# Performance work log

Hardware: AMD Instinct MI355X
Metric: run time of the kernel (lower is better)

Reference implementation:

```python
import jax, jax.numpy as jnp
import numpy as np

N, IN_DIM, OUT_DIM = 8192, 128, 64
NEG_INF = -9e15

def setup_inputs() -> dict:
    key = jax.random.key(0)
    k1, k2, k3, k4 = jax.random.split(key, 4)
    h = jax.random.normal(k1, (N, IN_DIM), dtype=jnp.float32)
    adj = jax.random.randint(k2, (N, N), 0, 2, dtype=jnp.int32)
    W = jax.random.normal(k3, (IN_DIM, OUT_DIM), dtype=jnp.float32) * (1.0 / np.sqrt(IN_DIM))
    a = jax.random.normal(k4, (2 * OUT_DIM,), dtype=jnp.float32)
    return {"h": h, "adj": adj, "W": W, "a": a}

def reference(h, adj, W, a):
    Wh = h @ W  # [N, F]
    F_ = Wh.shape[1]
    # additive decomposition of cat([Wh_i, Wh_j]) @ a == Wh_i@a1 + Wh_j@a2
    e_src = Wh @ a[:F_]   # [N]
    e_dst = Wh @ a[F_:]   # [N]
    e = jax.nn.leaky_relu(e_src[:, None] + e_dst[None, :], negative_slope=0.01)  # [N, N]
    attention = jnp.where(adj > 0, e, jnp.float32(NEG_INF))
    attention = jax.nn.softmax(attention, axis=1)
    h_prime = attention @ Wh  # [N, F]
    return jax.nn.elu(h_prime)
```

## Files before the change

### kernel.cpp

```cpp
#include <hip/hip_runtime.h>
#include <hip/hip_bf16.h>

typedef __attribute__((ext_vector_type(8))) short short8;
typedef __attribute__((ext_vector_type(4))) float f32x4;

#define NROW 8192
#define FDIM 64
#define INDIM 128
#define BM 128
#define SPLITS 16
#define NPANEL (NROW / BM)
#define MBOUND 48.0f
#define L2E 1.44269504f

static __device__ __forceinline__ unsigned short bfb(float x) {
  __hip_bfloat16 b = __float2bfloat16(x);
  return *reinterpret_cast<unsigned short*>(&b);
}
static __device__ __forceinline__ float b2f(unsigned int u16) {
  unsigned int x = u16 << 16;
  float f;
  __builtin_memcpy(&f, &x, 4);
  return f;
}
static __device__ __forceinline__ float lrelu(float x) { return fmaxf(x, 0.01f * x); }

__global__ __launch_bounds__(256) void k_wh(const float* __restrict__ h,
                                            const float* __restrict__ W,
                                            const float* __restrict__ a,
                                            __hip_bfloat16* __restrict__ WhT,
                                            float* __restrict__ s,
                                            float* __restrict__ d) {
  const int i = blockIdx.x * 4 + (threadIdx.x >> 6);
  const int f = threadIdx.x & 63;
  const float* hrow = h + (size_t)i * INDIM;
  float acc = 0.f;
#pragma unroll 8
  for (int k = 0; k < INDIM; ++k) acc = fmaf(hrow[k], W[k * FDIM + f], acc);
  WhT[(size_t)f * NROW + i] = __float2bfloat16(acc);
  float p1 = acc * a[f];
  float p2 = acc * a[FDIM + f];
#pragma unroll
  for (int m = 32; m; m >>= 1) {
    p1 += __shfl_xor(p1, m, 64);
    p2 += __shfl_xor(p2, m, 64);
  }
  if (f == 0) { s[i] = p1; d[i] = p2; }
}

__global__ __launch_bounds__(256, 4) void k_main(const int* __restrict__ adj,
                                                 const __hip_bfloat16* __restrict__ WhT,
                                                 const float* __restrict__ sArr,
                                                 const float* __restrict__ dArr,
                                                 unsigned int* __restrict__ accp,
                                                 float* __restrict__ Zp) {
  const int t = threadIdx.x;
  const int w = t >> 6, l = t & 63;
  const int lr = l & 15;
  const int lk = l >> 4;
  const int panel = blockIdx.x / SPLITS;
  const int split = blockIdx.x - panel * SPLITS;
  const int row0 = panel * BM + w * 32;
  const int jspan = NROW / SPLITS;
  const int j0 = split * jspan;
  const int nchunk = jspan / 64;

  const float s0 = sArr[row0 + lr];
  const float s1 = sArr[row0 + 16 + lr];
  const float sm0 = -lrelu(s0 + MBOUND) * L2E;
  const float sm1 = -lrelu(s1 + MBOUND) * L2E;

  f32x4 acc[2][4];
#pragma unroll
  for (int ri = 0; ri < 2; ++ri)
#pragma unroll
    for (int nf = 0; nf < 4; ++nf) acc[ri][nf] = (f32x4){0.f, 0.f, 0.f, 0.f};
  float z0 = 0.f, z1 = 0.f;

  const int* adjp = adj + (size_t)row0 * NROW + j0 + l;
  const float* dp = dArr + j0 + lk * 8;
  const __hip_bfloat16* bbase = WhT + (size_t)lr * NROW + j0 + lk * 8;

  for (int c = 0; c < nchunk; ++c) {
    const int off = c * 64;

    unsigned long long M0 = 0ull, M1 = 0ull;
    {
      int av[16];
#pragma unroll
      for (int r = 0; r < 16; ++r) av[r] = adjp[(size_t)r * NROW + off];
#pragma unroll
      for (int r = 0; r < 16; ++r) {
        unsigned long long b = __ballot(av[r] > 0);
        M0 = (lr == r) ? b : M0;
      }
#pragma unroll
      for (int r = 0; r < 16; ++r) av[r] = adjp[(size_t)(16 + r) * NROW + off];
#pragma unroll
      for (int r = 0; r < 16; ++r) {
        unsigned long long b = __ballot(av[r] > 0);
        M1 = (lr == r) ? b : M1;
      }
    }

#pragma unroll
    for (int ks = 0; ks < 2; ++ks) {
      const int jo = off + ks * 32;
      const unsigned int y0 = (unsigned int)(M0 >> (ks * 32 + lk * 8)) & 0xffu;
      const unsigned int y1 = (unsigned int)(M1 >> (ks * 32 + lk * 8)) & 0xffu;

      short8 b0 = *(const short8*)(bbase + jo);
      short8 b1 = *(const short8*)(bbase + jo + 16 * NROW);
      short8 b2 = *(const short8*)(bbase + jo + 32 * NROW);
      short8 b3 = *(const short8*)(bbase + jo + 48 * NROW);

      float dj[8];
      *(float4*)&dj[0] = *(const float4*)(dp + jo);
      *(float4*)&dj[4] = *(const float4*)(dp + jo + 4);

      short8 pa0, pa1;
#pragma unroll
      for (int q = 0; q < 8; ++q) {
        const float dq = dj[q];
        float e0 = exp2f(fmaf(lrelu(s0 + dq), L2E, sm0));
        float e1 = exp2f(fmaf(lrelu(s1 + dq), L2E, sm1));
        float w0 = ((y0 >> q) & 1u) ? e0 : 0.f;
        float w1 = ((y1 >> q) & 1u) ? e1 : 0.f;
        z0 += w0;
        z1 += w1;
        pa0[q] = (short)bfb(w0);
        pa1[q] = (short)bfb(w1);
      }

      acc[0][0] = __builtin_amdgcn_mfma_f32_16x16x32_bf16(pa0, b0, acc[0][0], 0, 0, 0);
      acc[0][1] = __builtin_amdgcn_mfma_f32_16x16x32_bf16(pa0, b1, acc[0][1], 0, 0, 0);
      acc[0][2] = __builtin_amdgcn_mfma_f32_16x16x32_bf16(pa0, b2, acc[0][2], 0, 0, 0);
      acc[0][3] = __builtin_amdgcn_mfma_f32_16x16x32_bf16(pa0, b3, acc[0][3], 0, 0, 0);
      acc[1][0] = __builtin_amdgcn_mfma_f32_16x16x32_bf16(pa1, b0, acc[1][0], 0, 0, 0);
      acc[1][1] = __builtin_amdgcn_mfma_f32_16x16x32_bf16(pa1, b1, acc[1][1], 0, 0, 0);
      acc[1][2] = __builtin_amdgcn_mfma_f32_16x16x32_bf16(pa1, b2, acc[1][2], 0, 0, 0);
      acc[1][3] = __builtin_amdgcn_mfma_f32_16x16x32_bf16(pa1, b3, acc[1][3], 0, 0, 0);
    }
  }

  z0 += __shfl_xor(z0, 16, 64);
  z0 += __shfl_xor(z0, 32, 64);
  z1 += __shfl_xor(z1, 16, 64);
  z1 += __shfl_xor(z1, 32, 64);
  if (l < 16) {
    Zp[(size_t)blockIdx.x * BM + w * 32 + lr] = z0;
    Zp[(size_t)blockIdx.x * BM + w * 32 + 16 + lr] = z1;
  }

  unsigned int* ab = accp + (size_t)blockIdx.x * 4096 + w * 1024 + l;
#pragma unroll
  for (int ri = 0; ri < 2; ++ri)
#pragma unroll
    for (int nf = 0; nf < 4; ++nf)
#pragma unroll
      for (int qp = 0; qp < 2; ++qp) {
        unsigned int pv = (unsigned int)bfb(acc[ri][nf][2 * qp]) |
                          ((unsigned int)bfb(acc[ri][nf][2 * qp + 1]) << 16);
        ab[ri * 512 + nf * 128 + qp * 64] = pv;
      }
}

__global__ __launch_bounds__(256) void k_combine(const unsigned int* __restrict__ accp,
                                                 const float* __restrict__ Zp,
                                                 float* __restrict__ out) {
  __shared__ float zsh[BM];
  const int panel = blockIdx.x >> 2;
  const int part = blockIdx.x & 3;
  const int t = threadIdx.x;

  if (t < BM) {
    float z = 0.f;
#pragma unroll
    for (int sp = 0; sp < SPLITS; ++sp)
      z += Zp[(size_t)(panel * SPLITS + sp) * BM + t];
    zsh[t] = z;
  }
  __syncthreads();

  const unsigned int* base = accp + (size_t)panel * SPLITS * 4096;
#pragma unroll
  for (int k = 0; k < 4; ++k) {
    const int D = part * 1024 + k * 256 + t;
    float sum0 = 0.f, sum1 = 0.f;
#pragma unroll
    for (int sp = 0; sp < SPLITS; ++sp) {
      unsigned int v = base[(size_t)sp * 4096 + D];
      sum0 += b2f(v & 0xffffu);
      sum1 += b2f(v >> 16);
    }
    const int w = D >> 10, ri = (D >> 9) & 1, nf = (D >> 7) & 3, qp = (D >> 6) & 1;
    const int lk = (D >> 4) & 3, lr = D & 15;
    const int row = w * 32 + ri * 16 + lk * 4 + 2 * qp;
    const int col = nf * 16 + lr;
    const float v0 = sum0 / zsh[row];
    const float v1 = sum1 / zsh[row + 1];
    out[(size_t)(panel * BM + row) * FDIM + col] = (v0 > 0.f) ? v0 : expm1f(v0);
    out[(size_t)(panel * BM + row + 1) * FDIM + col] = (v1 > 0.f) ? v1 : expm1f(v1);
  }
}

extern "C" void kernel_launch(void* const* d_in, const int* in_sizes, int n_in,
                              void* d_out, int out_size, void* d_ws, size_t ws_size,
                              hipStream_t stream) {
  const float* h = (const float*)d_in[0];
  const int* adj = (const int*)d_in[1];
  const float* W = (const float*)d_in[2];
  const float* a = (const float*)d_in[3];
  float* out = (float*)d_out;

  const int nblk = NPANEL * SPLITS;

  char* p = (char*)d_ws;
  __hip_bfloat16* WhT = (__hip_bfloat16*)p;
  float* s = (float*)(p + 1048576);
  float* d = (float*)(p + 1048576 + 32768);
  float* Zp = (float*)(p + 1048576 + 65536);
  unsigned int* accp =
      (unsigned int*)((char*)Zp + (size_t)nblk * BM * 4);

  hipLaunchKernelGGL(k_wh, dim3(NROW / 4), dim3(256), 0, stream, h, W, a, WhT, s, d);
  hipLaunchKernelGGL(k_main, dim3(nblk), dim3(256), 0, stream, adj, WhT, s, d, accp, Zp);
  hipLaunchKernelGGL(k_combine, dim3(NPANEL * 4), dim3(256), 0, stream, accp, Zp, out);
}
```

Baseline: 100.5 us.

## Load adjacency as int4 vectors and permute Wh/d columns to match

Each lane now loads four consecutive adjacency ints per row with a 16-byte load instead of one int, producing four ballot masks per row that each cover a strided set of columns. To make the mask bits line up with the MFMA K ordering, k_wh writes WhT and the d vector in a permuted column order within each 256-column group. The chunk loop is fully unrolled into two groups of 256 columns. The intent is fewer, wider adjacency loads on the dominant memory stream, at the cost of more live mask registers and a layout coupling between the two kernels.

```diff
diff --git a/kernel.cpp b/kernel.cpp
--- a/kernel.cpp
+++ b/kernel.cpp
@@ -25,6 +25,7 @@
 }
 static __device__ __forceinline__ float lrelu(float x) { return fmaxf(x, 0.01f * x); }
 
+
 __global__ __launch_bounds__(256) void k_wh(const float* __restrict__ h,
                                             const float* __restrict__ W,
                                             const float* __restrict__ a,
@@ -33,11 +34,12 @@
                                             float* __restrict__ d) {
   const int i = blockIdx.x * 4 + (threadIdx.x >> 6);
   const int f = threadIdx.x & 63;
+  const int vi = ((i >> 8) << 8) | ((i & 3) << 6) | ((i >> 2) & 63);
   const float* hrow = h + (size_t)i * INDIM;
   float acc = 0.f;
 #pragma unroll 8
   for (int k = 0; k < INDIM; ++k) acc = fmaf(hrow[k], W[k * FDIM + f], acc);
-  WhT[(size_t)f * NROW + i] = __float2bfloat16(acc);
+  WhT[(size_t)f * NROW + vi] = __float2bfloat16(acc);
   float p1 = acc * a[f];
   float p2 = acc * a[FDIM + f];
 #pragma unroll
@@ -45,7 +47,7 @@
     p1 += __shfl_xor(p1, m, 64);
     p2 += __shfl_xor(p2, m, 64);
   }
-  if (f == 0) { s[i] = p1; d[i] = p2; }
+  if (f == 0) { s[i] = p1; d[vi] = p2; }
 }
 
 __global__ __launch_bounds__(256, 4) void k_main(const int* __restrict__ adj,
@@ -63,7 +65,6 @@
   const int row0 = panel * BM + w * 32;
   const int jspan = NROW / SPLITS;
   const int j0 = split * jspan;
-  const int nchunk = jspan / 64;
 
   const float s0 = sArr[row0 + lr];
   const float s1 = sArr[row0 + 16 + lr];
@@ -77,69 +78,82 @@
     for (int nf = 0; nf < 4; ++nf) acc[ri][nf] = (f32x4){0.f, 0.f, 0.f, 0.f};
   float z0 = 0.f, z1 = 0.f;
 
-  const int* adjp = adj + (size_t)row0 * NROW + j0 + l;
+  const int4* apg = (const int4*)(adj + (size_t)row0 * NROW + j0) + l;
   const float* dp = dArr + j0 + lk * 8;
   const __hip_bfloat16* bbase = WhT + (size_t)lr * NROW + j0 + lk * 8;
 
-  for (int c = 0; c < nchunk; ++c) {
-    const int off = c * 64;
-
-    unsigned long long M0 = 0ull, M1 = 0ull;
-    {
-      int av[16];
-#pragma unroll
-      for (int r = 0; r < 16; ++r) av[r] = adjp[(size_t)r * NROW + off];
-#pragma unroll
-      for (int r = 0; r < 16; ++r) {
-        unsigned long long b = __ballot(av[r] > 0);
-        M0 = (lr == r) ? b : M0;
-      }
-#pragma unroll
-      for (int r = 0; r < 16; ++r) av[r] = adjp[(size_t)(16 + r) * NROW + off];
-#pragma unroll
-      for (int r = 0; r < 16; ++r) {
-        unsigned long long b = __ballot(av[r] > 0);
-        M1 = (lr == r) ? b : M1;
+#pragma unroll
+  for (int g = 0; g < 2; ++g) {
+    const int4* ap = apg + g * 64;
+
+    unsigned long long M0[4] = {0ull, 0ull, 0ull, 0ull};
+    unsigned long long M1[4] = {0ull, 0ull, 0ull, 0ull};
+#pragma unroll
+    for (int b = 0; b < 8; ++b) {
+      int4 av[4];
+#pragma unroll
+      for (int r = 0; r < 4; ++r) av[r] = ap[(size_t)(b * 4 + r) * (NROW / 4)];
+#pragma unroll
+      for (int r = 0; r < 4; ++r) {
+        const int row = b * 4 + r;
+        unsigned long long bb0 = __ballot(av[r].x > 0);
+        unsigned long long bb1 = __ballot(av[r].y > 0);
+        unsigned long long bb2 = __ballot(av[r].z > 0);
+        unsigned long long bb3 = __ballot(av[r].w > 0);
+        if (row < 16) {
+          M0[0] = (lr == row) ? bb0 : M0[0];
+          M0[1] = (lr == row) ? bb1 : M0[1];
+          M0[2] = (lr == row) ? bb2 : M0[2];
+          M0[3] = (lr == row) ? bb3 : M0[3];
+        } else {
+          M1[0] = (lr == row - 16) ? bb0 : M1[0];
+          M1[1] = (lr == row - 16) ? bb1 : M1[1];
+          M1[2] = (lr == row - 16) ? bb2 : M1[2];
+          M1[3] = (lr == row - 16) ? bb3 : M1[3];
+        }
       }
     }
 
 #pragma unroll
-    for (int ks = 0; ks < 2; ++ks) {
-      const int jo = off + ks * 32;
-      const unsigned int y0 = (unsigned int)(M0 >> (ks * 32 + lk * 8)) & 0xffu;
-      const unsigned int y1 = (unsigned int)(M1 >> (ks * 32 + lk * 8)) & 0xffu;
-
-      short8 b0 = *(const short8*)(bbase + jo);
-      short8 b1 = *(const short8*)(bbase + jo + 16 * NROW);
-      short8 b2 = *(const short8*)(bbase + jo + 32 * NROW);
-      short8 b3 = *(const short8*)(bbase + jo + 48 * NROW);
-
-      float dj[8];
-      *(float4*)&dj[0] = *(const float4*)(dp + jo);
-      *(float4*)&dj[4] = *(const float4*)(dp + jo + 4);
-
-      short8 pa0, pa1;
-#pragma unroll
-      for (int q = 0; q < 8; ++q) {
-        const float dq = dj[q];
-        float e0 = exp2f(fmaf(lrelu(s0 + dq), L2E, sm0));
-        float e1 = exp2f(fmaf(lrelu(s1 + dq), L2E, sm1));
-        float w0 = ((y0 >> q) & 1u) ? e0 : 0.f;
-        float w1 = ((y1 >> q) & 1u) ? e1 : 0.f;
-        z0 += w0;
-        z1 += w1;
-        pa0[q] = (short)bfb(w0);
-        pa1[q] = (short)bfb(w1);
+    for (int k = 0; k < 4; ++k) {
+#pragma unroll
+      for (int ks = 0; ks < 2; ++ks) {
+        const int jo = g * 256 + k * 64 + ks * 32;
+        const unsigned int y0 = (unsigned int)(M0[k] >> (ks * 32 + lk * 8)) & 0xffu;
+        const unsigned int y1 = (unsigned int)(M1[k] >> (ks * 32 + lk * 8)) & 0xffu;
+
+        short8 b0 = *(const short8*)(bbase + jo);
+        short8 b1 = *(const short8*)(bbase + jo + 16 * NROW);
+        short8 b2 = *(const short8*)(bbase + jo + 32 * NROW);
+        short8 b3 = *(const short8*)(bbase + jo + 48 * NROW);
+
+        float dj[8];
+        *(float4*)&dj[0] = *(const float4*)(dp + jo);
+        *(float4*)&dj[4] = *(const float4*)(dp + jo + 4);
+
+        short8 pa0, pa1;
+#pragma unroll
+        for (int q = 0; q < 8; ++q) {
+          const float dq = dj[q];
+          float e0 = exp2f(fmaf(lrelu(s0 + dq), L2E, sm0));
+          float e1 = exp2f(fmaf(lrelu(s1 + dq), L2E, sm1));
+          float w0 = ((y0 >> q) & 1u) ? e0 : 0.f;
+          float w1 = ((y1 >> q) & 1u) ? e1 : 0.f;
+          z0 += w0;
+          z1 += w1;
+          pa0[q] = (short)bfb(w0);
+          pa1[q] = (short)bfb(w1);
+        }
+
+        acc[0][0] = __builtin_amdgcn_mfma_f32_16x16x32_bf16(pa0, b0, acc[0][0], 0, 0, 0);
+        acc[0][1] = __builtin_amdgcn_mfma_f32_16x16x32_bf16(pa0, b1, acc[0][1], 0, 0, 0);
+        acc[0][2] = __builtin_amdgcn_mfma_f32_16x16x32_bf16(pa0, b2, acc[0][2], 0, 0, 0);
+        acc[0][3] = __builtin_amdgcn_mfma_f32_16x16x32_bf16(pa0, b3, acc[0][3], 0, 0, 0);
+        acc[1][0] = __builtin_amdgcn_mfma_f32_16x16x32_bf16(pa1, b0, acc[1][0], 0, 0, 0);
+        acc[1][1] = __builtin_amdgcn_mfma_f32_16x16x32_bf16(pa1, b1, acc[1][1], 0, 0, 0);
+        acc[1][2] = __builtin_amdgcn_mfma_f32_16x16x32_bf16(pa1, b2, acc[1][2], 0, 0, 0);
+        acc[1][3] = __builtin_amdgcn_mfma_f32_16x16x32_bf16(pa1, b3, acc[1][3], 0, 0, 0);
       }
-
-      acc[0][0] = __builtin_amdgcn_mfma_f32_16x16x32_bf16(pa0, b0, acc[0][0], 0, 0, 0);
-      acc[0][1] = __builtin_amdgcn_mfma_f32_16x16x32_bf16(pa0, b1, acc[0][1], 0, 0, 0);
-      acc[0][2] = __builtin_amdgcn_mfma_f32_16x16x32_bf16(pa0, b2, acc[0][2], 0, 0, 0);
-      acc[0][3] = __builtin_amdgcn_mfma_f32_16x16x32_bf16(pa0, b3, acc[0][3], 0, 0, 0);
-      acc[1][0] = __builtin_amdgcn_mfma_f32_16x16x32_bf16(pa1, b0, acc[1][0], 0, 0, 0);
-      acc[1][1] = __builtin_amdgcn_mfma_f32_16x16x32_bf16(pa1, b1, acc[1][1], 0, 0, 0);
-      acc[1][2] = __builtin_amdgcn_mfma_f32_16x16x32_bf16(pa1, b2, acc[1][2], 0, 0, 0);
-      acc[1][3] = __builtin_amdgcn_mfma_f32_16x16x32_bf16(pa1, b3, acc[1][3], 0, 0, 0);
     }
   }
 
@@ -194,9 +208,9 @@
       sum1 += b2f(v >> 16);
     }
     const int w = D >> 10, ri = (D >> 9) & 1, nf = (D >> 7) & 3, qp = (D >> 6) & 1;
-    const int lk = (D >> 4) & 3, lr = D & 15;
-    const int row = w * 32 + ri * 16 + lk * 4 + 2 * qp;
-    const int col = nf * 16 + lr;
+    const int lkD = (D >> 4) & 3, lrD = D & 15;
+    const int row = w * 32 + ri * 16 + lkD * 4 + 2 * qp;
+    const int col = nf * 16 + lrD;
     const float v0 = sum0 / zsh[row];
     const float v1 = sum1 / zsh[row + 1];
     out[(size_t)(panel * BM + row) * FDIM + col] = (v0 > 0.f) ? v0 : expm1f(v0);
```

New measurement: 123.0 us. 1.22x slower.
